# Kernel tuning notes

Hardware: AMD Instinct MI355X
Metric: run time of the kernel (lower is better)

## Reference

```python
import jax, jax.numpy as jnp
import numpy as np

N = 50000      # nodes
E = 800000     # edges (avg degree 16)
D_IN = 64
D_H = 128
D_OUT = 10
EPS = 1e-8


def setup_inputs() -> dict:
    key = jax.random.key(0)
    ks = jax.random.split(key, 6)
    x = jax.random.normal(ks[0], (N, D_IN), dtype=jnp.float32)
    edge_index = jax.random.randint(ks[1], (2, E), 0, N, dtype=jnp.int32)
    # weights act on homogeneous-augmented features (d_in + 1)
    W_self0 = jax.random.normal(ks[2], (D_IN + 1, D_H), jnp.float32) / np.sqrt(D_IN + 1)
    W_neigh0 = jax.random.normal(ks[3], (D_IN + 1, D_H), jnp.float32) / np.sqrt(D_IN + 1)
    W_self1 = jax.random.normal(ks[4], (D_H + 1, D_OUT), jnp.float32) / np.sqrt(D_H + 1)
    W_neigh1 = jax.random.normal(ks[5], (D_H + 1, D_OUT), jnp.float32) / np.sqrt(D_H + 1)
    return {"x": x, "edge_index": edge_index,
            "W_self0": W_self0, "W_neigh0": W_neigh0,
            "W_self1": W_self1, "W_neigh1": W_neigh1}


def _projective_sage_layer(h, src, dst, W_self, W_neigh, last):
    n = h.shape[0]
    # lift to projective (homogeneous) coordinates: append ones column
    hh = jnp.concatenate([h, jnp.ones((n, 1), h.dtype)], axis=1)  # [N, d+1]
    # mean-aggregate neighbor messages (irregular gather + segment-sum)
    msg_sum = jax.ops.segment_sum(hh[src], dst, num_segments=n)   # [N, d+1]
    deg = jax.ops.segment_sum(jnp.ones((src.shape[0],), h.dtype), dst, num_segments=n)
    neigh = msg_sum / jnp.maximum(deg, 1.0)[:, None]
    out = hh @ W_self + neigh @ W_neigh                           # [N, d_out]
    # projective normalization (points on unit sphere of projective space)
    out = out / (jnp.linalg.norm(out, axis=1, keepdims=True) + EPS)
    return out if last else jax.nn.relu(out)


def reference(x, edge_index, W_self0, W_neigh0, W_self1, W_neigh1):
    src, dst = edge_index[0], edge_index[1]
    h = _projective_sage_layer(x, src, dst, W_self0, W_neigh0, last=False)
    h = _projective_sage_layer(h, src, dst, W_self1, W_neigh1, last=True)
    return jax.nn.log_softmax(h, axis=1)
```

## Files before the change

### kernel.cpp

```cpp
#include <hip/hip_runtime.h>
#include <hip/hip_bf16.h>
#include <math.h>

#define EPSN 1e-8f
#define MAXBUCK 512

typedef __attribute__((ext_vector_type(8))) short short8;
typedef __attribute__((ext_vector_type(4))) float f32x4;

static __device__ __forceinline__ unsigned short f2bf(float f) {
    union { float f; unsigned int u; } v; v.f = f;
    unsigned int u = v.u;
    return (unsigned short)((u + 0x7fffu + ((u >> 16) & 1u)) >> 16);
}
static __device__ __forceinline__ float bf2f(unsigned short h) {
    union { unsigned int u; float f; } v; v.u = ((unsigned int)h) << 16;
    return v.f;
}

__global__ void bucket_hist(const int* __restrict__ dst, int* __restrict__ ghist,
                            int E, int nbuck) {
    __shared__ int h[MAXBUCK];
    for (int i = threadIdx.x; i < MAXBUCK; i += 256) h[i] = 0;
    __syncthreads();
    int CH = (E + gridDim.x - 1) / gridDim.x;
    int lo = blockIdx.x * CH, hi = min(E, lo + CH);
    for (int e = lo + (int)threadIdx.x; e < hi; e += 256) atomicAdd(&h[dst[e] >> 7], 1);
    __syncthreads();
    for (int i = threadIdx.x; i < nbuck; i += 256) if (h[i]) atomicAdd(&ghist[i], h[i]);
}

__global__ void bucket_scan(const int* __restrict__ ghist, int* __restrict__ boff,
                            int* __restrict__ bcur, int nbuck, int E,
                            int* __restrict__ row_ptr, int N) {
    __shared__ int bufa[MAXBUCK], bufb[MAXBUCK];
    int t = threadIdx.x;
    int v = (t < nbuck) ? ghist[t] : 0;
    bufa[t] = v;
    __syncthreads();
    int* cur = bufa; int* nxt = bufb;
    for (int off = 1; off < MAXBUCK; off <<= 1) {
        int x = cur[t];
        if (t >= off) x += cur[t - off];
        nxt[t] = x;
        __syncthreads();
        int* tmp = cur; cur = nxt; nxt = tmp;
    }
    int incl = cur[t];
    int excl = incl - v;
    if (t < nbuck) { boff[t] = excl; bcur[t] = excl; }
    if (t == nbuck - 1) boff[nbuck] = incl;
    if (t == 0) row_ptr[N] = E;
}

__global__ void bucket_scatter(const int* __restrict__ src, const int* __restrict__ dst,
                               int* __restrict__ bcur, unsigned int* __restrict__ pairs,
                               int E) {
    __shared__ int h[MAXBUCK];
    __shared__ int bs[MAXBUCK];
    for (int i = threadIdx.x; i < MAXBUCK; i += 256) h[i] = 0;
    __syncthreads();
    int CH = (E + gridDim.x - 1) / gridDim.x;
    int lo = blockIdx.x * CH, hi = min(E, lo + CH);
    for (int e = lo + (int)threadIdx.x; e < hi; e += 256) atomicAdd(&h[dst[e] >> 7], 1);
    __syncthreads();
    for (int i = threadIdx.x; i < MAXBUCK; i += 256) {
        int c = h[i];
        bs[i] = c ? atomicAdd(&bcur[i], c) : 0;
        h[i] = 0;
    }
    __syncthreads();
    for (int e = lo + (int)threadIdx.x; e < hi; e += 256) {
        int d = dst[e];
        int b = d >> 7;
        int idx = atomicAdd(&h[b], 1);
        pairs[bs[b] + idx] = (((unsigned int)(d & 127)) << 16) | (unsigned int)src[e];
    }
}

__global__ void csr_finalize(const unsigned int* __restrict__ pairs, const int* __restrict__ boff,
                             int* __restrict__ row_ptr, unsigned short* __restrict__ col,
                             int N) {
    __shared__ int lh[128], ls[128], lc[128];
    int b = blockIdx.x, t = threadIdx.x;
    int lo = boff[b], hi = boff[b + 1];
    for (int i = t; i < 128; i += 256) lh[i] = 0;
    __syncthreads();
    for (int e = lo + t; e < hi; e += 256) atomicAdd(&lh[pairs[e] >> 16], 1);
    __syncthreads();
    if (t < 128) {
        int v = lh[t];
        int incl = v;
#pragma unroll
        for (int off = 1; off < 64; off <<= 1) {
            int y = __shfl_up(incl, off);
            if ((t & 63) >= off) incl += y;
        }
        ls[t] = incl;
    }
    __syncthreads();
    if (t < 128) {
        int v = lh[t];
        int excl = ls[t] - v + ((t >= 64) ? ls[63] : 0);
        int node = b * 128 + t;
        if (node < N) row_ptr[node] = lo + excl;
        lc[t] = excl;
    }
    __syncthreads();
    for (int e = lo + t; e < hi; e += 256) {
        unsigned int p = pairs[e];
        int ld = p >> 16;
        int idx = atomicAdd(&lc[ld], 1);
        col[lo + idx] = (unsigned short)(p & 0xFFFFu);
    }
}

__global__ void prep_kernel(const float* __restrict__ Ws0, const float* __restrict__ Wn0,
                            const float* __restrict__ Ws1, const float* __restrict__ Wn1,
                            unsigned short* __restrict__ B0t, unsigned short* __restrict__ B1t,
                            float* __restrict__ bias) {
    int t = blockIdx.x * blockDim.x + threadIdx.x;
    if (t < 128 * 160) {
        int n = t / 160, k = t % 160;
        float v = 0.f;
        if (k < 65) v = Ws0[k * 128 + n];
        else if (k < 130) v = Wn0[(k - 65) * 128 + n];
        B0t[n * 160 + k] = f2bf(v);
    }
    int u = t - 128 * 160;
    if (u >= 0 && u < 32 * 128) {
        int c = u / 128, k = u % 128;
        float v = 0.f;
        if (c < 10) v = Ws1[k * 10 + c];
        else if (c < 20) v = Wn1[k * 10 + (c - 10)];
        B1t[c * 128 + k] = f2bf(v);
    }
    int w = t - 128 * 160 - 32 * 128;
    if (w >= 0 && w < 20) bias[w] = (w < 10) ? Ws1[128 * 10 + w] : Wn1[128 * 10 + (w - 10)];
}

__global__ void xconv_kernel(const float* __restrict__ x, unsigned short* __restrict__ A0, int N) {
    int u = blockIdx.x * blockDim.x + threadIdx.x;
    if (u >= N * 8) return;
    int n = u >> 3, s = u & 7;
    const float4* xp = (const float4*)(x + (size_t)n * 64 + s * 8);
    float4 v0 = xp[0], v1 = xp[1];
    short8 r;
    r[0] = (short)f2bf(v0.x); r[1] = (short)f2bf(v0.y);
    r[2] = (short)f2bf(v0.z); r[3] = (short)f2bf(v0.w);
    r[4] = (short)f2bf(v1.x); r[5] = (short)f2bf(v1.y);
    r[6] = (short)f2bf(v1.z); r[7] = (short)f2bf(v1.w);
    *(short8*)(&A0[(size_t)n * 160 + s * 8]) = r;
}

__global__ void agg0_kernel(const int* __restrict__ row_ptr, const unsigned short* __restrict__ col,
                            unsigned short* __restrict__ A0, int N) {
    int n = (int)((blockIdx.x * blockDim.x + threadIdx.x) >> 6);
    if (n >= N) return;
    int lane = threadIdx.x & 63;
    int rs = row_ptr[n], re = row_ptr[n + 1];
    float acc = 0.f;
    for (int base = rs; base < re; base += 64) {
        int cnt = min(64, re - base);
        int e = 0;
        if (base + lane < re) e = (int)col[base + lane];
        int j = 0;
        for (; j + 3 < cnt; j += 4) {
            int s0 = __shfl(e, j), s1 = __shfl(e, j + 1);
            int s2 = __shfl(e, j + 2), s3 = __shfl(e, j + 3);
            float v0 = bf2f(A0[(size_t)s0 * 160 + lane]);
            float v1 = bf2f(A0[(size_t)s1 * 160 + lane]);
            float v2 = bf2f(A0[(size_t)s2 * 160 + lane]);
            float v3 = bf2f(A0[(size_t)s3 * 160 + lane]);
            acc += v0; acc += v1; acc += v2; acc += v3;
        }
        for (; j < cnt; ++j) {
            int s = __shfl(e, j);
            acc += bf2f(A0[(size_t)s * 160 + lane]);
        }
    }
    float deg = (float)(re - rs);
    float scale = 1.0f / fmaxf(deg, 1.0f);
    unsigned short* row = A0 + (size_t)n * 160;
    row[65 + lane] = f2bf(acc * scale);
    if (lane == 0) row[64]  = 0x3F80;
    if (lane == 1) row[129] = f2bf(deg * scale);
    if (lane >= 2 && lane < 32) row[128 + lane] = 0;
}

__global__ void __launch_bounds__(256)
gemm0_kernel(const unsigned short* __restrict__ A0, const unsigned short* __restrict__ B0t,
             unsigned short* __restrict__ h1, int N) {
    __shared__ unsigned short As[64 * 168];
    __shared__ unsigned short Bs[128 * 168];
    int t = threadIdx.x, blk = blockIdx.x;
    for (int i = t; i < 128 * 20; i += 256) {
        int r = i / 20, c = i % 20;
        *(uint4*)(&Bs[r * 168 + c * 8]) = *(const uint4*)(&B0t[r * 160 + c * 8]);
    }
    for (int i = t; i < 64 * 20; i += 256) {
        int r = i / 20, c = i % 20;
        int gr = blk * 64 + r;
        uint4 v = {0, 0, 0, 0};
        if (gr < N) v = *(const uint4*)(&A0[(size_t)gr * 160 + c * 8]);
        *(uint4*)(&As[r * 168 + c * 8]) = v;
    }
    __syncthreads();

    int wave = t >> 6, lane = t & 63;
    int lo = lane & 15, hi = lane >> 4;
    f32x4 acc[8];
#pragma unroll
    for (int f = 0; f < 8; ++f) acc[f] = (f32x4){0.f, 0.f, 0.f, 0.f};

#pragma unroll
    for (int ks = 0; ks < 5; ++ks) {
        short8 a = *(const short8*)(&As[(wave * 16 + lo) * 168 + ks * 32 + hi * 8]);
#pragma unroll
        for (int f = 0; f < 8; ++f) {
            short8 b = *(const short8*)(&Bs[(f * 16 + lo) * 168 + ks * 32 + hi * 8]);
            acc[f] = __builtin_amdgcn_mfma_f32_16x16x32_bf16(a, b, acc[f], 0, 0, 0);
        }
    }
#pragma unroll
    for (int j = 0; j < 4; ++j) {
        float s = 0.f;
#pragma unroll
        for (int f = 0; f < 8; ++f) s += acc[f][j] * acc[f][j];
#pragma unroll
        for (int m = 1; m < 16; m <<= 1) s += __shfl_xor(s, m);
        float inv = 1.0f / (sqrtf(s) + EPSN);
        int gr = blk * 64 + wave * 16 + hi * 4 + j;
        if (gr < N) {
#pragma unroll
            for (int f = 0; f < 8; ++f)
                h1[(size_t)gr * 128 + f * 16 + lo] = f2bf(fmaxf(acc[f][j] * inv, 0.f));
        }
    }
}

__global__ void __launch_bounds__(256)
gemm1_kernel(const unsigned short* __restrict__ h1, const unsigned short* __restrict__ B1t,
             const float* __restrict__ bias, float* __restrict__ S, float* __restrict__ Q, int N) {
    __shared__ unsigned short As[128 * 136];
    __shared__ unsigned short Bs[32 * 136];
    int t = threadIdx.x, blk = blockIdx.x;
    for (int i = t; i < 32 * 16; i += 256) {
        int r = i / 16, c = i % 16;
        *(uint4*)(&Bs[r * 136 + c * 8]) = *(const uint4*)(&B1t[r * 128 + c * 8]);
    }
    for (int i = t; i < 128 * 16; i += 256) {
        int r = i / 16, c = i % 16;
        int gr = blk * 128 + r;
        uint4 v = {0, 0, 0, 0};
        if (gr < N) v = *(const uint4*)(&h1[(size_t)gr * 128 + c * 8]);
        *(uint4*)(&As[r * 136 + c * 8]) = v;
    }
    __syncthreads();

    int wave = t >> 6, lane = t & 63, lo = lane & 15, hi = lane >> 4;
    f32x4 acc[2][2];
#pragma unroll
    for (int m = 0; m < 2; ++m) { acc[m][0] = (f32x4){0,0,0,0}; acc[m][1] = (f32x4){0,0,0,0}; }

#pragma unroll
    for (int ks = 0; ks < 4; ++ks) {
        short8 b0 = *(const short8*)(&Bs[lo * 136 + ks * 32 + hi * 8]);
        short8 b1 = *(const short8*)(&Bs[(16 + lo) * 136 + ks * 32 + hi * 8]);
#pragma unroll
        for (int m = 0; m < 2; ++m) {
            short8 a = *(const short8*)(&As[(wave * 32 + m * 16 + lo) * 136 + ks * 32 + hi * 8]);
            acc[m][0] = __builtin_amdgcn_mfma_f32_16x16x32_bf16(a, b0, acc[m][0], 0, 0, 0);
            acc[m][1] = __builtin_amdgcn_mfma_f32_16x16x32_bf16(a, b1, acc[m][1], 0, 0, 0);
        }
    }
#pragma unroll
    for (int m = 0; m < 2; ++m)
#pragma unroll
        for (int j = 0; j < 4; ++j) {
            int gr = blk * 128 + wave * 32 + m * 16 + hi * 4 + j;
            if (gr < N) {
                float v0 = acc[m][0][j] + bias[lo];
                if (lo < 10) S[(size_t)gr * 10 + lo] = v0;
                else         Q[(size_t)gr * 10 + (lo - 10)] = v0;
                if (lo < 4)  Q[(size_t)gr * 10 + 6 + lo] = acc[m][1][j] + bias[16 + lo];
            }
        }
}

__global__ void final_kernel(const float* __restrict__ S, const float* __restrict__ Q,
                             const int* __restrict__ row_ptr, const unsigned short* __restrict__ col,
                             float* __restrict__ out, int N) {
    int n = blockIdx.x * blockDim.x + threadIdx.x;
    if (n >= N) return;
    int rs = row_ptr[n], re = row_ptr[n + 1];
    float q[10];
#pragma unroll
    for (int j = 0; j < 10; ++j) q[j] = 0.f;
    int e = rs;
    for (; e + 1 < re; e += 2) {
        const float* r0 = &Q[(size_t)col[e] * 10];
        const float* r1 = &Q[(size_t)col[e + 1] * 10];
#pragma unroll
        for (int j = 0; j < 10; ++j) q[j] += r0[j];
#pragma unroll
        for (int j = 0; j < 10; ++j) q[j] += r1[j];
    }
    if (e < re) {
        const float* r0 = &Q[(size_t)col[e] * 10];
#pragma unroll
        for (int j = 0; j < 10; ++j) q[j] += r0[j];
    }
    float deg = (float)(re - rs);
    float scale = 1.0f / fmaxf(deg, 1.0f);
    const float* Sr = &S[(size_t)n * 10];
    float p[10], ss = 0.f;
#pragma unroll
    for (int j = 0; j < 10; ++j) { p[j] = Sr[j] + q[j] * scale; ss = fmaf(p[j], p[j], ss); }
    float inv = 1.0f / (sqrtf(ss) + EPSN);
    float m = -INFINITY;
#pragma unroll
    for (int j = 0; j < 10; ++j) { p[j] *= inv; m = fmaxf(m, p[j]); }
    float se = 0.f;
#pragma unroll
    for (int j = 0; j < 10; ++j) se += expf(p[j] - m);
    float ls = logf(se) + m;
#pragma unroll
    for (int j = 0; j < 10; ++j) out[(size_t)n * 10 + j] = p[j] - ls;
}

extern "C" void kernel_launch(void* const* d_in, const int* in_sizes, int n_in,
                              void* d_out, int out_size, void* d_ws, size_t ws_size,
                              hipStream_t stream) {
    const float* x   = (const float*)d_in[0];
    const int*   ei  = (const int*)d_in[1];
    const float* Ws0 = (const float*)d_in[2];
    const float* Wn0 = (const float*)d_in[3];
    const float* Ws1 = (const float*)d_in[4];
    const float* Wn1 = (const float*)d_in[5];

    int N = in_sizes[0] / 64;
    int E = in_sizes[1] / 2;
    const int* src = ei;
    const int* dst = ei + E;
    int nbuck = (N + 127) / 128;

    char* ws = (char*)d_ws;
    size_t off = 0;
    unsigned short* A0   = (unsigned short*)(ws + off); off += (size_t)N * 160 * 2;
    unsigned short* h1   = (unsigned short*)(ws + off); off += (size_t)N * 128 * 2;
    float*          S    = (float*)(ws + off);          off += (size_t)N * 10 * 4;
    float*          Q    = (float*)(ws + off);          off += (size_t)N * 10 * 4;
    unsigned short* B0t  = (unsigned short*)(ws + off); off += 128 * 160 * 2;
    unsigned short* B1t  = (unsigned short*)(ws + off); off += 32 * 128 * 2;
    float*          bias = (float*)(ws + off);          off += 128;
    int*            rowp = (int*)(ws + off);            off += ((size_t)N + 4) * 4;
    unsigned short* colb = (unsigned short*)(ws + off); off += ((size_t)E + 8) * 2;
    unsigned int*   pairs= (unsigned int*)(ws + off);   off += (size_t)E * 4;
    int*            ghist= (int*)(ws + off);            off += MAXBUCK * 4;
    int*            boff = (int*)(ws + off);            off += (MAXBUCK + 1) * 4;
    int*            bcur = (int*)(ws + off);            off += MAXBUCK * 4;
    float* outp = (float*)d_out;

    hipMemsetAsync(ghist, 0, MAXBUCK * 4, stream);
    bucket_hist   <<<256, 256, 0, stream>>>(dst, ghist, E, nbuck);
    bucket_scan   <<<1, MAXBUCK, 0, stream>>>(ghist, boff, bcur, nbuck, E, rowp, N);
    bucket_scatter<<<256, 256, 0, stream>>>(src, dst, bcur, pairs, E);
    csr_finalize  <<<nbuck, 256, 0, stream>>>(pairs, boff, rowp, colb, N);

    int pt = 128 * 160 + 32 * 128 + 20;
    prep_kernel<<<(pt + 255) / 256, 256, 0, stream>>>(Ws0, Wn0, Ws1, Wn1, B0t, B1t, bias);

    xconv_kernel<<<(N * 8 + 255) / 256, 256, 0, stream>>>(x, A0, N);
    agg0_kernel <<<(N + 3) / 4, 256, 0, stream>>>(rowp, colb, A0, N);
    gemm0_kernel<<<(N + 63) / 64, 256, 0, stream>>>(A0, B0t, h1, N);
    gemm1_kernel<<<(N + 127) / 128, 256, 0, stream>>>(h1, B1t, bias, S, Q, N);
    final_kernel<<<(N + 255) / 256, 256, 0, stream>>>(S, Q, rowp, colb, outp, N);
}
```

Measured before the change: 180.6 us.

## Fuse preprocessing kernels, vectorize layer-0 gather, wave-parallel final aggregation

Merges the bucket histogram, weight prep and x conversion into one launch split by block index, removing two kernel launches. The layer-0 aggregation now has four 16-lane subgroups each gather a different edge, loading 4 bf16 values per lane, and reduces them with cross-lane shuffles. The A0 row layout is changed so the self and neighbour ones-columns sit at 128/129, and the weight prep is reordered to match. The final kernel uses a wavefront per node instead of a thread per node, reading Q padded to 16 floats and doing the norm and log-softmax with shuffles. The cost is many idle lanes in the final kernel and extra padding traffic.

```diff
diff --git a/kernel.cpp b/kernel.cpp
--- a/kernel.cpp
+++ b/kernel.cpp
@@ -18,129 +18,49 @@
     return v.f;
 }
 
-__global__ void bucket_hist(const int* __restrict__ dst, int* __restrict__ ghist,
-                            int E, int nbuck) {
-    __shared__ int h[MAXBUCK];
-    for (int i = threadIdx.x; i < MAXBUCK; i += 256) h[i] = 0;
-    __syncthreads();
-    int CH = (E + gridDim.x - 1) / gridDim.x;
-    int lo = blockIdx.x * CH, hi = min(E, lo + CH);
-    for (int e = lo + (int)threadIdx.x; e < hi; e += 256) atomicAdd(&h[dst[e] >> 7], 1);
-    __syncthreads();
-    for (int i = threadIdx.x; i < nbuck; i += 256) if (h[i]) atomicAdd(&ghist[i], h[i]);
-}
-
-__global__ void bucket_scan(const int* __restrict__ ghist, int* __restrict__ boff,
-                            int* __restrict__ bcur, int nbuck, int E,
-                            int* __restrict__ row_ptr, int N) {
-    __shared__ int bufa[MAXBUCK], bufb[MAXBUCK];
-    int t = threadIdx.x;
-    int v = (t < nbuck) ? ghist[t] : 0;
-    bufa[t] = v;
-    __syncthreads();
-    int* cur = bufa; int* nxt = bufb;
-    for (int off = 1; off < MAXBUCK; off <<= 1) {
-        int x = cur[t];
-        if (t >= off) x += cur[t - off];
-        nxt[t] = x;
+__global__ void fused_pre(const int* __restrict__ dst, int* __restrict__ ghist, int E, int nbuck,
+                          const float* __restrict__ Ws0, const float* __restrict__ Wn0,
+                          const float* __restrict__ Ws1, const float* __restrict__ Wn1,
+                          unsigned short* __restrict__ B0t, unsigned short* __restrict__ B1t,
+                          float* __restrict__ bias,
+                          const float* __restrict__ x, unsigned short* __restrict__ A0, int N,
+                          int histB, int prepB) {
+    int b = blockIdx.x;
+    if (b < histB) {
+        __shared__ int h[MAXBUCK];
+        for (int i = threadIdx.x; i < MAXBUCK; i += 256) h[i] = 0;
         __syncthreads();
-        int* tmp = cur; cur = nxt; nxt = tmp;
-    }
-    int incl = cur[t];
-    int excl = incl - v;
-    if (t < nbuck) { boff[t] = excl; bcur[t] = excl; }
-    if (t == nbuck - 1) boff[nbuck] = incl;
-    if (t == 0) row_ptr[N] = E;
-}
-
-__global__ void bucket_scatter(const int* __restrict__ src, const int* __restrict__ dst,
-                               int* __restrict__ bcur, unsigned int* __restrict__ pairs,
-                               int E) {
-    __shared__ int h[MAXBUCK];
-    __shared__ int bs[MAXBUCK];
-    for (int i = threadIdx.x; i < MAXBUCK; i += 256) h[i] = 0;
-    __syncthreads();
-    int CH = (E + gridDim.x - 1) / gridDim.x;
-    int lo = blockIdx.x * CH, hi = min(E, lo + CH);
-    for (int e = lo + (int)threadIdx.x; e < hi; e += 256) atomicAdd(&h[dst[e] >> 7], 1);
-    __syncthreads();
-    for (int i = threadIdx.x; i < MAXBUCK; i += 256) {
-        int c = h[i];
-        bs[i] = c ? atomicAdd(&bcur[i], c) : 0;
-        h[i] = 0;
-    }
-    __syncthreads();
-    for (int e = lo + (int)threadIdx.x; e < hi; e += 256) {
-        int d = dst[e];
-        int b = d >> 7;
-        int idx = atomicAdd(&h[b], 1);
-        pairs[bs[b] + idx] = (((unsigned int)(d & 127)) << 16) | (unsigned int)src[e];
-    }
-}
-
-__global__ void csr_finalize(const unsigned int* __restrict__ pairs, const int* __restrict__ boff,
-                             int* __restrict__ row_ptr, unsigned short* __restrict__ col,
-                             int N) {
-    __shared__ int lh[128], ls[128], lc[128];
-    int b = blockIdx.x, t = threadIdx.x;
-    int lo = boff[b], hi = boff[b + 1];
-    for (int i = t; i < 128; i += 256) lh[i] = 0;
-    __syncthreads();
-    for (int e = lo + t; e < hi; e += 256) atomicAdd(&lh[pairs[e] >> 16], 1);
-    __syncthreads();
-    if (t < 128) {
-        int v = lh[t];
-        int incl = v;
-#pragma unroll
-        for (int off = 1; off < 64; off <<= 1) {
-            int y = __shfl_up(incl, off);
-            if ((t & 63) >= off) incl += y;
-        }
-        ls[t] = incl;
-    }
-    __syncthreads();
-    if (t < 128) {
-        int v = lh[t];
-        int excl = ls[t] - v + ((t >= 64) ? ls[63] : 0);
-        int node = b * 128 + t;
-        if (node < N) row_ptr[node] = lo + excl;
-        lc[t] = excl;
-    }
-    __syncthreads();
-    for (int e = lo + t; e < hi; e += 256) {
-        unsigned int p = pairs[e];
-        int ld = p >> 16;
-        int idx = atomicAdd(&lc[ld], 1);
-        col[lo + idx] = (unsigned short)(p & 0xFFFFu);
-    }
-}
-
-__global__ void prep_kernel(const float* __restrict__ Ws0, const float* __restrict__ Wn0,
-                            const float* __restrict__ Ws1, const float* __restrict__ Wn1,
-                            unsigned short* __restrict__ B0t, unsigned short* __restrict__ B1t,
-                            float* __restrict__ bias) {
-    int t = blockIdx.x * blockDim.x + threadIdx.x;
-    if (t < 128 * 160) {
-        int n = t / 160, k = t % 160;
-        float v = 0.f;
-        if (k < 65) v = Ws0[k * 128 + n];
-        else if (k < 130) v = Wn0[(k - 65) * 128 + n];
-        B0t[n * 160 + k] = f2bf(v);
-    }
-    int u = t - 128 * 160;
-    if (u >= 0 && u < 32 * 128) {
-        int c = u / 128, k = u % 128;
-        float v = 0.f;
-        if (c < 10) v = Ws1[k * 10 + c];
-        else if (c < 20) v = Wn1[k * 10 + (c - 10)];
-        B1t[c * 128 + k] = f2bf(v);
-    }
-    int w = t - 128 * 160 - 32 * 128;
-    if (w >= 0 && w < 20) bias[w] = (w < 10) ? Ws1[128 * 10 + w] : Wn1[128 * 10 + (w - 10)];
-}
-
-__global__ void xconv_kernel(const float* __restrict__ x, unsigned short* __restrict__ A0, int N) {
-    int u = blockIdx.x * blockDim.x + threadIdx.x;
+        int CH = (E + histB - 1) / histB;
+        int lo = b * CH, hi = min(E, lo + CH);
+        for (int e = lo + (int)threadIdx.x; e < hi; e += 256) atomicAdd(&h[dst[e] >> 7], 1);
+        __syncthreads();
+        for (int i = threadIdx.x; i < nbuck; i += 256) if (h[i]) atomicAdd(&ghist[i], h[i]);
+        return;
+    }
+    if (b < histB + prepB) {
+        int t = (b - histB) * 256 + threadIdx.x;
+        if (t < 128 * 160) {
+            int n = t / 160, k = t % 160;
+            float v = 0.f;
+            if (k < 64) v = Ws0[k * 128 + n];
+            else if (k < 128) v = Wn0[(k - 64) * 128 + n];
+            else if (k == 128) v = Ws0[64 * 128 + n];
+            else if (k == 129) v = Wn0[64 * 128 + n];
+            B0t[n * 160 + k] = f2bf(v);
+        }
+        int u = t - 128 * 160;
+        if (u >= 0 && u < 32 * 128) {
+            int c = u / 128, k = u % 128;
+            float v = 0.f;
+            if (c < 10) v = Ws1[k * 10 + c];
+            else if (c < 20) v = Wn1[k * 10 + (c - 10)];
+            B1t[c * 128 + k] = f2bf(v);
+        }
+        int w = t - 128 * 160 - 32 * 128;
+        if (w >= 0 && w < 20) bias[w] = (w < 10) ? Ws1[128 * 10 + w] : Wn1[128 * 10 + (w - 10)];
+        return;
+    }
+    int u = (b - histB - prepB) * 256 + threadIdx.x;
     if (u >= N * 8) return;
     int n = u >> 3, s = u & 7;
     const float4* xp = (const float4*)(x + (size_t)n * 64 + s * 8);
@@ -153,39 +73,127 @@
     *(short8*)(&A0[(size_t)n * 160 + s * 8]) = r;
 }
 
+__global__ void bucket_scan(const int* __restrict__ ghist, int* __restrict__ boff,
+                            int* __restrict__ bcur, int nbuck, int E,
+                            int* __restrict__ row_ptr, int N) {
+    __shared__ int bufa[MAXBUCK], bufb[MAXBUCK];
+    int t = threadIdx.x;
+    int v = (t < nbuck) ? ghist[t] : 0;
+    bufa[t] = v;
+    __syncthreads();
+    int* cur = bufa; int* nxt = bufb;
+    for (int off = 1; off < MAXBUCK; off <<= 1) {
+        int xv = cur[t];
+        if (t >= off) xv += cur[t - off];
+        nxt[t] = xv;
+        __syncthreads();
+        int* tmp = cur; cur = nxt; nxt = tmp;
+    }
+    int incl = cur[t];
+    int excl = incl - v;
+    if (t < nbuck) { boff[t] = excl; bcur[t] = excl; }
+    if (t == nbuck - 1) boff[nbuck] = incl;
+    if (t == 0) row_ptr[N] = E;
+}
+
+__global__ void bucket_scatter(const int* __restrict__ src, const int* __restrict__ dst,
+                               int* __restrict__ bcur, unsigned int* __restrict__ pairs,
+                               int E) {
+    __shared__ int h[MAXBUCK];
+    __shared__ int bs[MAXBUCK];
+    for (int i = threadIdx.x; i < MAXBUCK; i += 256) h[i] = 0;
+    __syncthreads();
+    int CH = (E + gridDim.x - 1) / gridDim.x;
+    int lo = blockIdx.x * CH, hi = min(E, lo + CH);
+    for (int e = lo + (int)threadIdx.x; e < hi; e += 256) atomicAdd(&h[dst[e] >> 7], 1);
+    __syncthreads();
+    for (int i = threadIdx.x; i < MAXBUCK; i += 256) {
+        int c = h[i];
+        bs[i] = c ? atomicAdd(&bcur[i], c) : 0;
+        h[i] = 0;
+    }
+    __syncthreads();
+    for (int e = lo + (int)threadIdx.x; e < hi; e += 256) {
+        int d = dst[e];
+        int b = d >> 7;
+        int idx = atomicAdd(&h[b], 1);
+        pairs[bs[b] + idx] = (((unsigned int)(d & 127)) << 16) | (unsigned int)src[e];
+    }
+}
+
+__global__ void csr_finalize(const unsigned int* __restrict__ pairs, const int* __restrict__ boff,
+                             int* __restrict__ row_ptr, unsigned short* __restrict__ col,
+                             int N) {
+    __shared__ int lh[128], ls[128], lc[128];
+    int b = blockIdx.x, t = threadIdx.x;
+    int lo = boff[b], hi = boff[b + 1];
+    for (int i = t; i < 128; i += 256) lh[i] = 0;
+    __syncthreads();
+    for (int e = lo + t; e < hi; e += 256) atomicAdd(&lh[pairs[e] >> 16], 1);
+    __syncthreads();
+    if (t < 128) {
+        int v = lh[t];
+        int incl = v;
+#pragma unroll
+        for (int off = 1; off < 64; off <<= 1) {
+            int y = __shfl_up(incl, off);
+            if ((t & 63) >= off) incl += y;
+        }
+        ls[t] = incl;
+    }
+    __syncthreads();
+    if (t < 128) {
+        int v = lh[t];
+        int excl = ls[t] - v + ((t >= 64) ? ls[63] : 0);
+        int node = b * 128 + t;
+        if (node < N) row_ptr[node] = lo + excl;
+        lc[t] = excl;
+    }
+    __syncthreads();
+    for (int e = lo + t; e < hi; e += 256) {
+        unsigned int p = pairs[e];
+        int ld = p >> 16;
+        int idx = atomicAdd(&lc[ld], 1);
+        col[lo + idx] = (unsigned short)(p & 0xFFFFu);
+    }
+}
+
 __global__ void agg0_kernel(const int* __restrict__ row_ptr, const unsigned short* __restrict__ col,
                             unsigned short* __restrict__ A0, int N) {
     int n = (int)((blockIdx.x * blockDim.x + threadIdx.x) >> 6);
     if (n >= N) return;
     int lane = threadIdx.x & 63;
+    int sub = lane >> 4, f = lane & 15;
     int rs = row_ptr[n], re = row_ptr[n + 1];
-    float acc = 0.f;
-    for (int base = rs; base < re; base += 64) {
-        int cnt = min(64, re - base);
-        int e = 0;
-        if (base + lane < re) e = (int)col[base + lane];
-        int j = 0;
-        for (; j + 3 < cnt; j += 4) {
-            int s0 = __shfl(e, j), s1 = __shfl(e, j + 1);
-            int s2 = __shfl(e, j + 2), s3 = __shfl(e, j + 3);
-            float v0 = bf2f(A0[(size_t)s0 * 160 + lane]);
-            float v1 = bf2f(A0[(size_t)s1 * 160 + lane]);
-            float v2 = bf2f(A0[(size_t)s2 * 160 + lane]);
-            float v3 = bf2f(A0[(size_t)s3 * 160 + lane]);
-            acc += v0; acc += v1; acc += v2; acc += v3;
-        }
-        for (; j < cnt; ++j) {
-            int s = __shfl(e, j);
-            acc += bf2f(A0[(size_t)s * 160 + lane]);
-        }
-    }
+    float a0 = 0.f, a1 = 0.f, a2 = 0.f, a3 = 0.f;
+    for (int base = rs; base < re; base += 4) {
+        int ei = base + sub;
+        uint2 v = {0u, 0u};
+        if (ei < re) {
+            int s = (int)col[ei];
+            v = *(const uint2*)(&A0[(size_t)s * 160 + f * 4]);
+        }
+        a0 += bf2f((unsigned short)(v.x & 0xFFFFu));
+        a1 += bf2f((unsigned short)(v.x >> 16));
+        a2 += bf2f((unsigned short)(v.y & 0xFFFFu));
+        a3 += bf2f((unsigned short)(v.y >> 16));
+    }
+    a0 += __shfl_xor(a0, 16); a0 += __shfl_xor(a0, 32);
+    a1 += __shfl_xor(a1, 16); a1 += __shfl_xor(a1, 32);
+    a2 += __shfl_xor(a2, 16); a2 += __shfl_xor(a2, 32);
+    a3 += __shfl_xor(a3, 16); a3 += __shfl_xor(a3, 32);
     float deg = (float)(re - rs);
     float scale = 1.0f / fmaxf(deg, 1.0f);
     unsigned short* row = A0 + (size_t)n * 160;
-    row[65 + lane] = f2bf(acc * scale);
-    if (lane == 0) row[64]  = 0x3F80;
-    if (lane == 1) row[129] = f2bf(deg * scale);
-    if (lane >= 2 && lane < 32) row[128 + lane] = 0;
+    if (sub == 0) {
+        uint2 o;
+        o.x = ((unsigned int)f2bf(a1 * scale) << 16) | f2bf(a0 * scale);
+        o.y = ((unsigned int)f2bf(a3 * scale) << 16) | f2bf(a2 * scale);
+        *(uint2*)(&row[64 + f * 4]) = o;
+    } else if (sub == 1) {
+        unsigned int w = (f == 0) ? ((((unsigned int)f2bf(deg * scale)) << 16) | 0x3F80u) : 0u;
+        *(unsigned int*)(&row[128 + f * 2]) = w;
+    }
 }
 
 __global__ void __launch_bounds__(256)
@@ -241,7 +249,7 @@
 
 __global__ void __launch_bounds__(256)
 gemm1_kernel(const unsigned short* __restrict__ h1, const unsigned short* __restrict__ B1t,
-             const float* __restrict__ bias, float* __restrict__ S, float* __restrict__ Q, int N) {
+             const float* __restrict__ bias, float* __restrict__ S, float* __restrict__ Qp, int N) {
     __shared__ unsigned short As[128 * 136];
     __shared__ unsigned short Bs[32 * 136];
     int t = threadIdx.x, blk = blockIdx.x;
@@ -282,51 +290,55 @@
             if (gr < N) {
                 float v0 = acc[m][0][j] + bias[lo];
                 if (lo < 10) S[(size_t)gr * 10 + lo] = v0;
-                else         Q[(size_t)gr * 10 + (lo - 10)] = v0;
-                if (lo < 4)  Q[(size_t)gr * 10 + 6 + lo] = acc[m][1][j] + bias[16 + lo];
+                else         Qp[(size_t)gr * 16 + (lo - 10)] = v0;
+                if (lo < 4)       Qp[(size_t)gr * 16 + 6 + lo] = acc[m][1][j] + bias[16 + lo];
+                else if (lo < 10) Qp[(size_t)gr * 16 + 6 + lo] = 0.f;
             }
         }
 }
 
-__global__ void final_kernel(const float* __restrict__ S, const float* __restrict__ Q,
+__global__ void final_kernel(const float* __restrict__ S, const float* __restrict__ Qp,
                              const int* __restrict__ row_ptr, const unsigned short* __restrict__ col,
                              float* __restrict__ out, int N) {
-    int n = blockIdx.x * blockDim.x + threadIdx.x;
+    int n = (int)((blockIdx.x * blockDim.x + threadIdx.x) >> 6);
     if (n >= N) return;
+    int lane = threadIdx.x & 63;
+    int sub = lane >> 4, f = lane & 15;
     int rs = row_ptr[n], re = row_ptr[n + 1];
-    float q[10];
-#pragma unroll
-    for (int j = 0; j < 10; ++j) q[j] = 0.f;
-    int e = rs;
-    for (; e + 1 < re; e += 2) {
-        const float* r0 = &Q[(size_t)col[e] * 10];
-        const float* r1 = &Q[(size_t)col[e + 1] * 10];
-#pragma unroll
-        for (int j = 0; j < 10; ++j) q[j] += r0[j];
-#pragma unroll
-        for (int j = 0; j < 10; ++j) q[j] += r1[j];
-    }
-    if (e < re) {
-        const float* r0 = &Q[(size_t)col[e] * 10];
-#pragma unroll
-        for (int j = 0; j < 10; ++j) q[j] += r0[j];
-    }
+    float qx = 0.f, qy = 0.f;
+    for (int base = rs; base < re; base += 4) {
+        int ei = base + sub;
+        if (ei < re && f < 8) {
+            int c = (int)col[ei];
+            float2 v = *(const float2*)(&Qp[(size_t)c * 16 + f * 2]);
+            qx += v.x; qy += v.y;
+        }
+    }
+    qx += __shfl_xor(qx, 16); qx += __shfl_xor(qx, 32);
+    qy += __shfl_xor(qy, 16); qy += __shfl_xor(qy, 32);
     float deg = (float)(re - rs);
     float scale = 1.0f / fmaxf(deg, 1.0f);
-    const float* Sr = &S[(size_t)n * 10];
-    float p[10], ss = 0.f;
-#pragma unroll
-    for (int j = 0; j < 10; ++j) { p[j] = Sr[j] + q[j] * scale; ss = fmaf(p[j], p[j], ss); }
+    float px = 0.f, py = 0.f;
+    if (f < 5) {
+        px = S[(size_t)n * 10 + 2 * f]     + qx * scale;
+        py = S[(size_t)n * 10 + 2 * f + 1] + qy * scale;
+    }
+    float ss = px * px + py * py;
+    ss += __shfl_xor(ss, 1); ss += __shfl_xor(ss, 2);
+    ss += __shfl_xor(ss, 4); ss += __shfl_xor(ss, 8);
     float inv = 1.0f / (sqrtf(ss) + EPSN);
-    float m = -INFINITY;
-#pragma unroll
-    for (int j = 0; j < 10; ++j) { p[j] *= inv; m = fmaxf(m, p[j]); }
-    float se = 0.f;
-#pragma unroll
-    for (int j = 0; j < 10; ++j) se += expf(p[j] - m);
-    float ls = logf(se) + m;
-#pragma unroll
-    for (int j = 0; j < 10; ++j) out[(size_t)n * 10 + j] = p[j] - ls;
+    px *= inv; py *= inv;
+    float mx = (f < 5) ? fmaxf(px, py) : -INFINITY;
+    mx = fmaxf(mx, __shfl_xor(mx, 1)); mx = fmaxf(mx, __shfl_xor(mx, 2));
+    mx = fmaxf(mx, __shfl_xor(mx, 4)); mx = fmaxf(mx, __shfl_xor(mx, 8));
+    float se = (f < 5) ? (expf(px - mx) + expf(py - mx)) : 0.f;
+    se += __shfl_xor(se, 1); se += __shfl_xor(se, 2);
+    se += __shfl_xor(se, 4); se += __shfl_xor(se, 8);
+    float ls = logf(se) + mx;
+    if (sub == 0 && f < 5) {
+        out[(size_t)n * 10 + 2 * f]     = px - ls;
+        out[(size_t)n * 10 + 2 * f + 1] = py - ls;
+    }
 }
 
 extern "C" void kernel_launch(void* const* d_in, const int* in_sizes, int n_in,
@@ -350,7 +362,7 @@
     unsigned short* A0   = (unsigned short*)(ws + off); off += (size_t)N * 160 * 2;
     unsigned short* h1   = (unsigned short*)(ws + off); off += (size_t)N * 128 * 2;
     float*          S    = (float*)(ws + off);          off += (size_t)N * 10 * 4;
-    float*          Q    = (float*)(ws + off);          off += (size_t)N * 10 * 4;
+    float*          Qp   = (float*)(ws + off);          off += (size_t)N * 16 * 4;
     unsigned short* B0t  = (unsigned short*)(ws + off); off += 128 * 160 * 2;
     unsigned short* B1t  = (unsigned short*)(ws + off); off += 32 * 128 * 2;
     float*          bias = (float*)(ws + off);          off += 128;
@@ -362,18 +374,19 @@
     int*            bcur = (int*)(ws + off);            off += MAXBUCK * 4;
     float* outp = (float*)d_out;
 
+    int histB = 256;
+    int prepB = (128 * 160 + 32 * 128 + 20 + 255) / 256;
+    int xcvB  = (N * 8 + 255) / 256;
+
     hipMemsetAsync(ghist, 0, MAXBUCK * 4, stream);
-    bucket_hist   <<<256, 256, 0, stream>>>(dst, ghist, E, nbuck);
+    fused_pre<<<histB + prepB + xcvB, 256, 0, stream>>>(
+        dst, ghist, E, nbuck, Ws0, Wn0, Ws1, Wn1, B0t, B1t, bias, x, A0, N, histB, prepB);
     bucket_scan   <<<1, MAXBUCK, 0, stream>>>(ghist, boff, bcur, nbuck, E, rowp, N);
     bucket_scatter<<<256, 256, 0, stream>>>(src, dst, bcur, pairs, E);
     csr_finalize  <<<nbuck, 256, 0, stream>>>(pairs, boff, rowp, colb, N);
 
-    int pt = 128 * 160 + 32 * 128 + 20;
-    prep_kernel<<<(pt + 255) / 256, 256, 0, stream>>>(Ws0, Wn0, Ws1, Wn1, B0t, B1t, bias);
-
-    xconv_kernel<<<(N * 8 + 255) / 256, 256, 0, stream>>>(x, A0, N);
     agg0_kernel <<<(N + 3) / 4, 256, 0, stream>>>(rowp, colb, A0, N);
     gemm0_kernel<<<(N + 63) / 64, 256, 0, stream>>>(A0, B0t, h1, N);
-    gemm1_kernel<<<(N + 127) / 128, 256, 0, stream>>>(h1, B1t, bias, S, Q, N);
-    final_kernel<<<(N + 255) / 256, 256, 0, stream>>>(S, Q, rowp, colb, outp, N);
-}
+    gemm1_kernel<<<(N + 127) / 128, 256, 0, stream>>>(h1, B1t, bias, S, Qp, N);
+    final_kernel<<<(N + 3) / 4, 256, 0, stream>>>(S, Qp, rowp, colb, outp, N);
+}
```

Measured after the change: 202.8 us. +12.3%, slower.

## Fuse histogram, weight prep and x conversion; pad Q rows for vector gathers

Applied to the files above, without the earlier changes.

Merges the bucket histogram, weight repacking and x-to-bf16 conversion into one launch with block-range dispatch, removing two kernel launches and letting these independent jobs run concurrently. The layer-0 A0 layout is changed so the neighbor mean starts at column 64 (aligned), with the bias/degree columns packed at 128-129 and written as 32-bit stores. The Q buffer is padded to 16 floats per row so the final kernel gathers neighbor rows with float4/float2 loads instead of scalar loads. This costs extra memory for the padded Q and zero writes for the padding.

```diff
diff --git a/kernel.cpp b/kernel.cpp
--- a/kernel.cpp
+++ b/kernel.cpp
@@ -17,130 +17,53 @@
     union { unsigned int u; float f; } v; v.u = ((unsigned int)h) << 16;
     return v.f;
 }
-
-__global__ void bucket_hist(const int* __restrict__ dst, int* __restrict__ ghist,
-                            int E, int nbuck) {
-    __shared__ int h[MAXBUCK];
-    for (int i = threadIdx.x; i < MAXBUCK; i += 256) h[i] = 0;
-    __syncthreads();
-    int CH = (E + gridDim.x - 1) / gridDim.x;
-    int lo = blockIdx.x * CH, hi = min(E, lo + CH);
-    for (int e = lo + (int)threadIdx.x; e < hi; e += 256) atomicAdd(&h[dst[e] >> 7], 1);
-    __syncthreads();
-    for (int i = threadIdx.x; i < nbuck; i += 256) if (h[i]) atomicAdd(&ghist[i], h[i]);
-}
-
-__global__ void bucket_scan(const int* __restrict__ ghist, int* __restrict__ boff,
-                            int* __restrict__ bcur, int nbuck, int E,
-                            int* __restrict__ row_ptr, int N) {
-    __shared__ int bufa[MAXBUCK], bufb[MAXBUCK];
-    int t = threadIdx.x;
-    int v = (t < nbuck) ? ghist[t] : 0;
-    bufa[t] = v;
-    __syncthreads();
-    int* cur = bufa; int* nxt = bufb;
-    for (int off = 1; off < MAXBUCK; off <<= 1) {
-        int x = cur[t];
-        if (t >= off) x += cur[t - off];
-        nxt[t] = x;
+static __device__ __forceinline__ unsigned int pk2(float a, float b) {
+    return (((unsigned int)f2bf(b)) << 16) | (unsigned int)f2bf(a);
+}
+
+__global__ void fused_pre(const int* __restrict__ dst, int* __restrict__ ghist, int E, int nbuck,
+                          const float* __restrict__ Ws0, const float* __restrict__ Wn0,
+                          const float* __restrict__ Ws1, const float* __restrict__ Wn1,
+                          unsigned short* __restrict__ B0t, unsigned short* __restrict__ B1t,
+                          float* __restrict__ bias,
+                          const float* __restrict__ x, unsigned short* __restrict__ A0, int N,
+                          int histB, int prepB) {
+    int b = blockIdx.x;
+    if (b < histB) {
+        __shared__ int h[MAXBUCK];
+        for (int i = threadIdx.x; i < MAXBUCK; i += 256) h[i] = 0;
         __syncthreads();
-        int* tmp = cur; cur = nxt; nxt = tmp;
-    }
-    int incl = cur[t];
-    int excl = incl - v;
-    if (t < nbuck) { boff[t] = excl; bcur[t] = excl; }
-    if (t == nbuck - 1) boff[nbuck] = incl;
-    if (t == 0) row_ptr[N] = E;
-}
-
-__global__ void bucket_scatter(const int* __restrict__ src, const int* __restrict__ dst,
-                               int* __restrict__ bcur, unsigned int* __restrict__ pairs,
-                               int E) {
-    __shared__ int h[MAXBUCK];
-    __shared__ int bs[MAXBUCK];
-    for (int i = threadIdx.x; i < MAXBUCK; i += 256) h[i] = 0;
-    __syncthreads();
-    int CH = (E + gridDim.x - 1) / gridDim.x;
-    int lo = blockIdx.x * CH, hi = min(E, lo + CH);
-    for (int e = lo + (int)threadIdx.x; e < hi; e += 256) atomicAdd(&h[dst[e] >> 7], 1);
-    __syncthreads();
-    for (int i = threadIdx.x; i < MAXBUCK; i += 256) {
-        int c = h[i];
-        bs[i] = c ? atomicAdd(&bcur[i], c) : 0;
-        h[i] = 0;
-    }
-    __syncthreads();
-    for (int e = lo + (int)threadIdx.x; e < hi; e += 256) {
-        int d = dst[e];
-        int b = d >> 7;
-        int idx = atomicAdd(&h[b], 1);
-        pairs[bs[b] + idx] = (((unsigned int)(d & 127)) << 16) | (unsigned int)src[e];
-    }
-}
-
-__global__ void csr_finalize(const unsigned int* __restrict__ pairs, const int* __restrict__ boff,
-                             int* __restrict__ row_ptr, unsigned short* __restrict__ col,
-                             int N) {
-    __shared__ int lh[128], ls[128], lc[128];
-    int b = blockIdx.x, t = threadIdx.x;
-    int lo = boff[b], hi = boff[b + 1];
-    for (int i = t; i < 128; i += 256) lh[i] = 0;
-    __syncthreads();
-    for (int e = lo + t; e < hi; e += 256) atomicAdd(&lh[pairs[e] >> 16], 1);
-    __syncthreads();
-    if (t < 128) {
-        int v = lh[t];
-        int incl = v;
-#pragma unroll
-        for (int off = 1; off < 64; off <<= 1) {
-            int y = __shfl_up(incl, off);
-            if ((t & 63) >= off) incl += y;
-        }
-        ls[t] = incl;
-    }
-    __syncthreads();
-    if (t < 128) {
-        int v = lh[t];
-        int excl = ls[t] - v + ((t >= 64) ? ls[63] : 0);
-        int node = b * 128 + t;
-        if (node < N) row_ptr[node] = lo + excl;
-        lc[t] = excl;
-    }
-    __syncthreads();
-    for (int e = lo + t; e < hi; e += 256) {
-        unsigned int p = pairs[e];
-        int ld = p >> 16;
-        int idx = atomicAdd(&lc[ld], 1);
-        col[lo + idx] = (unsigned short)(p & 0xFFFFu);
-    }
-}
-
-__global__ void prep_kernel(const float* __restrict__ Ws0, const float* __restrict__ Wn0,
-                            const float* __restrict__ Ws1, const float* __restrict__ Wn1,
-                            unsigned short* __restrict__ B0t, unsigned short* __restrict__ B1t,
-                            float* __restrict__ bias) {
-    int t = blockIdx.x * blockDim.x + threadIdx.x;
-    if (t < 128 * 160) {
-        int n = t / 160, k = t % 160;
-        float v = 0.f;
-        if (k < 65) v = Ws0[k * 128 + n];
-        else if (k < 130) v = Wn0[(k - 65) * 128 + n];
-        B0t[n * 160 + k] = f2bf(v);
-    }
-    int u = t - 128 * 160;
-    if (u >= 0 && u < 32 * 128) {
-        int c = u / 128, k = u % 128;
-        float v = 0.f;
-        if (c < 10) v = Ws1[k * 10 + c];
-        else if (c < 20) v = Wn1[k * 10 + (c - 10)];
-        B1t[c * 128 + k] = f2bf(v);
-    }
-    int w = t - 128 * 160 - 32 * 128;
-    if (w >= 0 && w < 20) bias[w] = (w < 10) ? Ws1[128 * 10 + w] : Wn1[128 * 10 + (w - 10)];
-}
-
-__global__ void xconv_kernel(const float* __restrict__ x, unsigned short* __restrict__ A0, int N) {
-    int u = blockIdx.x * blockDim.x + threadIdx.x;
+        int CH = (E + histB - 1) / histB;
+        int lo = b * CH, hi = min(E, lo + CH);
+        for (int e = lo + (int)threadIdx.x; e < hi; e += 256) atomicAdd(&h[dst[e] >> 7], 1);
+        __syncthreads();
+        for (int i = threadIdx.x; i < nbuck; i += 256) if (h[i]) atomicAdd(&ghist[i], h[i]);
+        return;
+    }
+    if (b < histB + prepB) {
+        int t = (b - histB) * 256 + threadIdx.x;
+        if (t < 128 * 160) {
+            int n = t / 160, k = t % 160;
+            float v = 0.f;
+            if (k < 64) v = Ws0[k * 128 + n];
+            else if (k < 128) v = Wn0[(k - 64) * 128 + n];
+            else if (k == 128) v = Ws0[64 * 128 + n];
+            else if (k == 129) v = Wn0[64 * 128 + n];
+            B0t[n * 160 + k] = f2bf(v);
+        }
+        int u = t - 128 * 160;
+        if (u >= 0 && u < 32 * 128) {
+            int c = u / 128, k = u % 128;
+            float v = 0.f;
+            if (c < 10) v = Ws1[k * 10 + c];
+            else if (c < 20) v = Wn1[k * 10 + (c - 10)];
+            B1t[c * 128 + k] = f2bf(v);
+        }
+        int w = t - 128 * 160 - 32 * 128;
+        if (w >= 0 && w < 20) bias[w] = (w < 10) ? Ws1[128 * 10 + w] : Wn1[128 * 10 + (w - 10)];
+        return;
+    }
+    int u = (b - histB - prepB) * 256 + threadIdx.x;
     if (u >= N * 8) return;
     int n = u >> 3, s = u & 7;
     const float4* xp = (const float4*)(x + (size_t)n * 64 + s * 8);
@@ -151,6 +74,91 @@
     r[4] = (short)f2bf(v1.x); r[5] = (short)f2bf(v1.y);
     r[6] = (short)f2bf(v1.z); r[7] = (short)f2bf(v1.w);
     *(short8*)(&A0[(size_t)n * 160 + s * 8]) = r;
+}
+
+__global__ void bucket_scan(const int* __restrict__ ghist, int* __restrict__ boff,
+                            int* __restrict__ bcur, int nbuck, int E,
+                            int* __restrict__ row_ptr, int N) {
+    __shared__ int bufa[MAXBUCK], bufb[MAXBUCK];
+    int t = threadIdx.x;
+    int v = (t < nbuck) ? ghist[t] : 0;
+    bufa[t] = v;
+    __syncthreads();
+    int* cur = bufa; int* nxt = bufb;
+    for (int off = 1; off < MAXBUCK; off <<= 1) {
+        int xv = cur[t];
+        if (t >= off) xv += cur[t - off];
+        nxt[t] = xv;
+        __syncthreads();
+        int* tmp = cur; cur = nxt; nxt = tmp;
+    }
+    int incl = cur[t];
+    int excl = incl - v;
+    if (t < nbuck) { boff[t] = excl; bcur[t] = excl; }
+    if (t == nbuck - 1) boff[nbuck] = incl;
+    if (t == 0) row_ptr[N] = E;
+}
+
+__global__ void bucket_scatter(const int* __restrict__ src, const int* __restrict__ dst,
+                               int* __restrict__ bcur, unsigned int* __restrict__ pairs,
+                               int E) {
+    __shared__ int h[MAXBUCK];
+    __shared__ int bs[MAXBUCK];
+    for (int i = threadIdx.x; i < MAXBUCK; i += 256) h[i] = 0;
+    __syncthreads();
+    int CH = (E + gridDim.x - 1) / gridDim.x;
+    int lo = blockIdx.x * CH, hi = min(E, lo + CH);
+    for (int e = lo + (int)threadIdx.x; e < hi; e += 256) atomicAdd(&h[dst[e] >> 7], 1);
+    __syncthreads();
+    for (int i = threadIdx.x; i < MAXBUCK; i += 256) {
+        int c = h[i];
+        bs[i] = c ? atomicAdd(&bcur[i], c) : 0;
+        h[i] = 0;
+    }
+    __syncthreads();
+    for (int e = lo + (int)threadIdx.x; e < hi; e += 256) {
+        int d = dst[e];
+        int b = d >> 7;
+        int idx = atomicAdd(&h[b], 1);
+        pairs[bs[b] + idx] = (((unsigned int)(d & 127)) << 16) | (unsigned int)src[e];
+    }
+}
+
+__global__ void csr_finalize(const unsigned int* __restrict__ pairs, const int* __restrict__ boff,
+                             int* __restrict__ row_ptr, unsigned short* __restrict__ col,
+                             int N) {
+    __shared__ int lh[128], ls[128], lc[128];
+    int b = blockIdx.x, t = threadIdx.x;
+    int lo = boff[b], hi = boff[b + 1];
+    for (int i = t; i < 128; i += 256) lh[i] = 0;
+    __syncthreads();
+    for (int e = lo + t; e < hi; e += 256) atomicAdd(&lh[pairs[e] >> 16], 1);
+    __syncthreads();
+    if (t < 128) {
+        int v = lh[t];
+        int incl = v;
+#pragma unroll
+        for (int off = 1; off < 64; off <<= 1) {
+            int y = __shfl_up(incl, off);
+            if ((t & 63) >= off) incl += y;
+        }
+        ls[t] = incl;
+    }
+    __syncthreads();
+    if (t < 128) {
+        int v = lh[t];
+        int excl = ls[t] - v + ((t >= 64) ? ls[63] : 0);
+        int node = b * 128 + t;
+        if (node < N) row_ptr[node] = lo + excl;
+        lc[t] = excl;
+    }
+    __syncthreads();
+    for (int e = lo + t; e < hi; e += 256) {
+        unsigned int p = pairs[e];
+        int ld = p >> 16;
+        int idx = atomicAdd(&lc[ld], 1);
+        col[lo + idx] = (unsigned short)(p & 0xFFFFu);
+    }
 }
 
 __global__ void agg0_kernel(const int* __restrict__ row_ptr, const unsigned short* __restrict__ col,
@@ -182,10 +190,9 @@
     float deg = (float)(re - rs);
     float scale = 1.0f / fmaxf(deg, 1.0f);
     unsigned short* row = A0 + (size_t)n * 160;
-    row[65 + lane] = f2bf(acc * scale);
-    if (lane == 0) row[64]  = 0x3F80;
-    if (lane == 1) row[129] = f2bf(deg * scale);
-    if (lane >= 2 && lane < 32) row[128 + lane] = 0;
+    row[64 + lane] = f2bf(acc * scale);
+    if (lane == 0) *(unsigned int*)(&row[128]) = pk2(1.0f, deg * scale);
+    if (lane >= 1 && lane < 16) *(unsigned int*)(&row[128 + lane * 2]) = 0u;
 }
 
 __global__ void __launch_bounds__(256)
@@ -241,7 +248,7 @@
 
 __global__ void __launch_bounds__(256)
 gemm1_kernel(const unsigned short* __restrict__ h1, const unsigned short* __restrict__ B1t,
-             const float* __restrict__ bias, float* __restrict__ S, float* __restrict__ Q, int N) {
+             const float* __restrict__ bias, float* __restrict__ S, float* __restrict__ Qp, int N) {
     __shared__ unsigned short As[128 * 136];
     __shared__ unsigned short Bs[32 * 136];
     int t = threadIdx.x, blk = blockIdx.x;
@@ -282,41 +289,55 @@
             if (gr < N) {
                 float v0 = acc[m][0][j] + bias[lo];
                 if (lo < 10) S[(size_t)gr * 10 + lo] = v0;
-                else         Q[(size_t)gr * 10 + (lo - 10)] = v0;
-                if (lo < 4)  Q[(size_t)gr * 10 + 6 + lo] = acc[m][1][j] + bias[16 + lo];
+                else         Qp[(size_t)gr * 16 + (lo - 10)] = v0;
+                if (lo < 4)       Qp[(size_t)gr * 16 + 6 + lo] = acc[m][1][j] + bias[16 + lo];
+                else if (lo < 10) Qp[(size_t)gr * 16 + 6 + lo] = 0.f;
             }
         }
 }
 
-__global__ void final_kernel(const float* __restrict__ S, const float* __restrict__ Q,
+__global__ void final_kernel(const float* __restrict__ S, const float* __restrict__ Qp,
                              const int* __restrict__ row_ptr, const unsigned short* __restrict__ col,
                              float* __restrict__ out, int N) {
     int n = blockIdx.x * blockDim.x + threadIdx.x;
     if (n >= N) return;
     int rs = row_ptr[n], re = row_ptr[n + 1];
-    float q[10];
-#pragma unroll
-    for (int j = 0; j < 10; ++j) q[j] = 0.f;
+    float q0 = 0.f, q1 = 0.f, q2 = 0.f, q3 = 0.f, q4 = 0.f;
+    float q5 = 0.f, q6 = 0.f, q7 = 0.f, q8 = 0.f, q9 = 0.f;
     int e = rs;
     for (; e + 1 < re; e += 2) {
-        const float* r0 = &Q[(size_t)col[e] * 10];
-        const float* r1 = &Q[(size_t)col[e + 1] * 10];
-#pragma unroll
-        for (int j = 0; j < 10; ++j) q[j] += r0[j];
-#pragma unroll
-        for (int j = 0; j < 10; ++j) q[j] += r1[j];
+        int c0 = (int)col[e], c1 = (int)col[e + 1];
+        const float4* r0 = (const float4*)(&Qp[(size_t)c0 * 16]);
+        const float4* r1 = (const float4*)(&Qp[(size_t)c1 * 16]);
+        float4 a0 = r0[0], b0 = r0[1];
+        float2 t0 = *(const float2*)(&Qp[(size_t)c0 * 16 + 8]);
+        float4 a1 = r1[0], b1 = r1[1];
+        float2 t1 = *(const float2*)(&Qp[(size_t)c1 * 16 + 8]);
+        q0 += a0.x + a1.x; q1 += a0.y + a1.y; q2 += a0.z + a1.z; q3 += a0.w + a1.w;
+        q4 += b0.x + b1.x; q5 += b0.y + b1.y; q6 += b0.z + b1.z; q7 += b0.w + b1.w;
+        q8 += t0.x + t1.x; q9 += t0.y + t1.y;
     }
     if (e < re) {
-        const float* r0 = &Q[(size_t)col[e] * 10];
-#pragma unroll
-        for (int j = 0; j < 10; ++j) q[j] += r0[j];
+        int c0 = (int)col[e];
+        const float4* r0 = (const float4*)(&Qp[(size_t)c0 * 16]);
+        float4 a0 = r0[0], b0 = r0[1];
+        float2 t0 = *(const float2*)(&Qp[(size_t)c0 * 16 + 8]);
+        q0 += a0.x; q1 += a0.y; q2 += a0.z; q3 += a0.w;
+        q4 += b0.x; q5 += b0.y; q6 += b0.z; q7 += b0.w;
+        q8 += t0.x; q9 += t0.y;
     }
     float deg = (float)(re - rs);
     float scale = 1.0f / fmaxf(deg, 1.0f);
     const float* Sr = &S[(size_t)n * 10];
-    float p[10], ss = 0.f;
-#pragma unroll
-    for (int j = 0; j < 10; ++j) { p[j] = Sr[j] + q[j] * scale; ss = fmaf(p[j], p[j], ss); }
+    float p[10];
+    p[0] = Sr[0] + q0 * scale; p[1] = Sr[1] + q1 * scale;
+    p[2] = Sr[2] + q2 * scale; p[3] = Sr[3] + q3 * scale;
+    p[4] = Sr[4] + q4 * scale; p[5] = Sr[5] + q5 * scale;
+    p[6] = Sr[6] + q6 * scale; p[7] = Sr[7] + q7 * scale;
+    p[8] = Sr[8] + q8 * scale; p[9] = Sr[9] + q9 * scale;
+    float ss = 0.f;
+#pragma unroll
+    for (int j = 0; j < 10; ++j) ss = fmaf(p[j], p[j], ss);
     float inv = 1.0f / (sqrtf(ss) + EPSN);
     float m = -INFINITY;
 #pragma unroll
@@ -350,7 +371,7 @@
     unsigned short* A0   = (unsigned short*)(ws + off); off += (size_t)N * 160 * 2;
     unsigned short* h1   = (unsigned short*)(ws + off); off += (size_t)N * 128 * 2;
     float*          S    = (float*)(ws + off);          off += (size_t)N * 10 * 4;
-    float*          Q    = (float*)(ws + off);          off += (size_t)N * 10 * 4;
+    float*          Qp   = (float*)(ws + off);          off += (size_t)N * 16 * 4;
     unsigned short* B0t  = (unsigned short*)(ws + off); off += 128 * 160 * 2;
     unsigned short* B1t  = (unsigned short*)(ws + off); off += 32 * 128 * 2;
     float*          bias = (float*)(ws + off);          off += 128;
@@ -362,18 +383,19 @@
     int*            bcur = (int*)(ws + off);            off += MAXBUCK * 4;
     float* outp = (float*)d_out;
 
+    int histB = 256;
+    int prepB = (128 * 160 + 32 * 128 + 20 + 255) / 256;
+    int xcvB  = (N * 8 + 255) / 256;
+
     hipMemsetAsync(ghist, 0, MAXBUCK * 4, stream);
-    bucket_hist   <<<256, 256, 0, stream>>>(dst, ghist, E, nbuck);
+    fused_pre<<<histB + prepB + xcvB, 256, 0, stream>>>(
+        dst, ghist, E, nbuck, Ws0, Wn0, Ws1, Wn1, B0t, B1t, bias, x, A0, N, histB, prepB);
     bucket_scan   <<<1, MAXBUCK, 0, stream>>>(ghist, boff, bcur, nbuck, E, rowp, N);
     bucket_scatter<<<256, 256, 0, stream>>>(src, dst, bcur, pairs, E);
     csr_finalize  <<<nbuck, 256, 0, stream>>>(pairs, boff, rowp, colb, N);
 
-    int pt = 128 * 160 + 32 * 128 + 20;
-    prep_kernel<<<(pt + 255) / 256, 256, 0, stream>>>(Ws0, Wn0, Ws1, Wn1, B0t, B1t, bias);
-
-    xconv_kernel<<<(N * 8 + 255) / 256, 256, 0, stream>>>(x, A0, N);
     agg0_kernel <<<(N + 3) / 4, 256, 0, stream>>>(rowp, colb, A0, N);
     gemm0_kernel<<<(N + 63) / 64, 256, 0, stream>>>(A0, B0t, h1, N);
-    gemm1_kernel<<<(N + 127) / 128, 256, 0, stream>>>(h1, B1t, bias, S, Q, N);
-    final_kernel<<<(N + 255) / 256, 256, 0, stream>>>(S, Q, rowp, colb, outp, N);
-}
+    gemm1_kernel<<<(N + 127) / 128, 256, 0, stream>>>(h1, B1t, bias, S, Qp, N);
+    final_kernel<<<(N + 255) / 256, 256, 0, stream>>>(S, Qp, rowp, colb, outp, N);
+}
```

New measurement: 184.3 us. 1.02x slower.
